# Kernel optimization log

Measured on AMD Instinct MI355X. Metric: run time of the kernel, lower is better.

Reference implementation:

```python
import jax, jax.numpy as jnp
import numpy as np

N = 100000
E = 800000

def elu(x):
    return jnp.where(x > 0, x, jnp.expm1(x))

def transformer_conv(x, src, dst, ea, Wq, bq, Wk, bk, Wv, bv, We, Ws, bs, heads, ch):
    # PyG TransformerConv (concat=True, root_weight=True, beta=False, eval so dropout off)
    n = x.shape[0]
    q = (x @ Wq + bq).reshape(n, heads, ch)
    k = (x @ Wk + bk).reshape(n, heads, ch)
    v = (x @ Wv + bv).reshape(n, heads, ch)
    e = (ea @ We).reshape(-1, heads, ch)            # [E,H,C], lin_edge has no bias
    kj = k[src] + e                                  # [E,H,C]
    logits = (q[dst] * kj).sum(-1) / jnp.sqrt(jnp.float32(ch))  # [E,H]
    # segment softmax over incoming edges of each dst node
    m = jax.ops.segment_max(logits, dst, num_segments=n)
    ex = jnp.exp(logits - m[dst])
    denom = jax.ops.segment_sum(ex, dst, num_segments=n)
    alpha = ex / denom[dst]                          # [E,H]
    msg = alpha[..., None] * (v[src] + e)            # [E,H,C]
    agg = jax.ops.segment_sum(msg, dst, num_segments=n).reshape(n, heads * ch)
    return agg + x @ Ws + bs                         # skip connection (lin_skip)

def setup_inputs() -> dict:
    key = jax.random.key(0)
    ks = jax.random.split(key, 32)
    def rn(k, shape, scale=0.1):
        return jax.random.normal(k, shape, dtype=jnp.float32) * scale
    d = {}
    d['x'] = jax.random.normal(ks[0], (N, 23), dtype=jnp.float32)
    d['edge_index'] = jax.random.randint(ks[1], (2, E), 0, N, dtype=jnp.int32)
    d['edge_attr'] = jax.random.normal(ks[2], (E, 7), dtype=jnp.float32)
    d['linA_w'] = rn(ks[3], (23, 23)); d['linA_b'] = jnp.zeros((23,), jnp.float32)
    d['linB_w'] = rn(ks[4], (23, 23)); d['linB_b'] = jnp.zeros((23,), jnp.float32)
    # conv1: in=23, heads=8, out=24 -> 192
    d['q1_w'] = rn(ks[5], (23, 192)); d['q1_b'] = jnp.zeros((192,), jnp.float32)
    d['k1_w'] = rn(ks[6], (23, 192)); d['k1_b'] = jnp.zeros((192,), jnp.float32)
    d['v1_w'] = rn(ks[7], (23, 192)); d['v1_b'] = jnp.zeros((192,), jnp.float32)
    d['e1_w'] = rn(ks[8], (7, 192))
    d['s1_w'] = rn(ks[9], (23, 192)); d['s1_b'] = jnp.zeros((192,), jnp.float32)
    # conv4: in=192, heads=8, out=8 -> 64
    d['q2_w'] = rn(ks[10], (192, 64)); d['q2_b'] = jnp.zeros((64,), jnp.float32)
    d['k2_w'] = rn(ks[11], (192, 64)); d['k2_b'] = jnp.zeros((64,), jnp.float32)
    d['v2_w'] = rn(ks[12], (192, 64)); d['v2_b'] = jnp.zeros((64,), jnp.float32)
    d['e2_w'] = rn(ks[13], (7, 64))
    d['s2_w'] = rn(ks[14], (192, 64)); d['s2_b'] = jnp.zeros((64,), jnp.float32)
    d['lin1_w'] = rn(ks[15], (64, 20)); d['lin1_b'] = jnp.zeros((20,), jnp.float32)
    d['lin2_w'] = rn(ks[16], (20, 1)); d['lin2_b'] = jnp.zeros((1,), jnp.float32)
    return d

def reference(x, edge_index, edge_attr,
              linA_w, linA_b, linB_w, linB_b,
              q1_w, q1_b, k1_w, k1_b, v1_w, v1_b, e1_w, s1_w, s1_b,
              q2_w, q2_b, k2_w, k2_b, v2_w, v2_b, e2_w, s2_w, s2_b,
              lin1_w, lin1_b, lin2_w, lin2_b):
    src, dst = edge_index[0], edge_index[1]
    h = elu(x @ linA_w + linA_b)
    h = elu(h @ linB_w + linB_b)
    h = transformer_conv(h, src, dst, edge_attr, q1_w, q1_b, k1_w, k1_b, v1_w, v1_b, e1_w, s1_w, s1_b, 8, 24)
    h = elu(h)
    h = transformer_conv(h, src, dst, edge_attr, q2_w, q2_b, k2_w, k2_b, v2_w, v2_b, e2_w, s2_w, s2_b, 8, 8)
    h = elu(h)
    h = elu(h @ lin1_w + lin1_b)
    return h @ lin2_w + lin2_b
```

## Files before the change

kernel.cpp:

```cpp
#include <hip/hip_runtime.h>
#include <math.h>


__device__ __forceinline__ float elu_f(float x) {
    return x > 0.f ? x : expm1f(x);
}


__global__ void mlp_kernel(const float* __restrict__ x,
                           const float* __restrict__ A, const float* __restrict__ ab,
                           const float* __restrict__ B, const float* __restrict__ bb,
                           float* __restrict__ out, int n) {
    __shared__ float sA[23 * 23], sB[23 * 23], sa[23], sb[23];
    for (int t = threadIdx.x; t < 23 * 23; t += blockDim.x) { sA[t] = A[t]; sB[t] = B[t]; }
    if (threadIdx.x < 23) { sa[threadIdx.x] = ab[threadIdx.x]; sb[threadIdx.x] = bb[threadIdx.x]; }
    __syncthreads();
    int i = blockIdx.x * blockDim.x + threadIdx.x;
    if (i >= n) return;
    float xi[23], h1[23];
    #pragma unroll
    for (int j = 0; j < 23; j++) xi[j] = x[(size_t)i * 23 + j];
    #pragma unroll
    for (int o = 0; o < 23; o++) {
        float acc = sa[o];
        #pragma unroll
        for (int j = 0; j < 23; j++) acc = fmaf(xi[j], sA[j * 23 + o], acc);
        h1[o] = elu_f(acc);
    }
    #pragma unroll
    for (int o = 0; o < 23; o++) {
        float acc = sb[o];
        #pragma unroll
        for (int j = 0; j < 23; j++) acc = fmaf(h1[j], sB[j * 23 + o], acc);
        out[(size_t)i * 23 + o] = elu_f(acc);
    }
}

template<int IN, int Kc, int OUTW, int M, int TY>
__global__ void proj_tiled_kernel(const float* __restrict__ in, int n,
    const float* __restrict__ W0, const float* __restrict__ b0, float* __restrict__ o0,
    const float* __restrict__ W1, const float* __restrict__ b1, float* __restrict__ o1,
    const float* __restrict__ W2, const float* __restrict__ b2, float* __restrict__ o2,
    const float* __restrict__ W3, const float* __restrict__ b3, float* __restrict__ o3) {
    constexpr int WTOT = M * OUTW;
    constexpr int CG   = WTOT / 8;
    constexpr int BN   = TY * 4;
    constexpr int SAW  = BN + 4;
    constexpr int NT   = CG * TY;
    static_assert(IN % Kc == 0, "Kc must divide IN");
    static_assert(WTOT % 8 == 0 && OUTW % 4 == 0, "col alignment");
    __shared__ float sA[Kc][SAW];
    __shared__ float sB[Kc][WTOT];

    const int tid = threadIdx.x;
    const int tx = tid % CG;
    const int ty = tid / CG;
    const int node0 = blockIdx.x * BN;

    const int colA = tx * 4;
    const int colB = WTOT / 2 + tx * 4;
    const int matA = colA / OUTW, ccA = colA % OUTW;
    const int matB = colB / OUTW, ccB = colB % OUTW;
    const float* bA = (matA == 0 ? b0 : matA == 1 ? b1 : matA == 2 ? b2 : b3);
    const float* bB = (matB == 0 ? b0 : matB == 1 ? b1 : matB == 2 ? b2 : b3);
    float*       oA = (matA == 0 ? o0 : matA == 1 ? o1 : matA == 2 ? o2 : o3);
    float*       oB = (matB == 0 ? o0 : matB == 1 ? o1 : matB == 2 ? o2 : o3);

    float acc[4][8];
    #pragma unroll
    for (int i = 0; i < 4; i++) {
        #pragma unroll
        for (int c = 0; c < 4; c++) { acc[i][c] = bA[ccA + c]; acc[i][4 + c] = bB[ccB + c]; }
    }

    for (int k0 = 0; k0 < IN; k0 += Kc) {
        for (int t = tid; t < Kc * BN; t += NT) {
            int j = t / BN, nn = t - j * BN;
            int g = node0 + nn;
            sA[j][nn] = (g < n) ? in[(size_t)g * IN + k0 + j] : 0.f;
        }
        for (int t = tid; t < Kc * WTOT; t += NT) {
            int j = t / WTOT, c = t - j * WTOT;
            int m = c / OUTW, cm = c - m * OUTW;
            const float* Wp = (m == 0 ? W0 : m == 1 ? W1 : m == 2 ? W2 : W3);
            sB[j][c] = Wp[(size_t)(k0 + j) * OUTW + cm];
        }
        __syncthreads();
        #pragma unroll 8
        for (int j = 0; j < Kc; j++) {
            float4 a  = *(const float4*)&sA[j][ty * 4];
            float4 v0 = *(const float4*)&sB[j][colA];
            float4 v1 = *(const float4*)&sB[j][colB];
            float av[4] = {a.x, a.y, a.z, a.w};
            float bv[8] = {v0.x, v0.y, v0.z, v0.w, v1.x, v1.y, v1.z, v1.w};
            #pragma unroll
            for (int i = 0; i < 4; i++)
                #pragma unroll
                for (int c = 0; c < 8; c++)
                    acc[i][c] = fmaf(av[i], bv[c], acc[i][c]);
        }
        __syncthreads();
    }

    #pragma unroll
    for (int i = 0; i < 4; i++) {
        int g = node0 + ty * 4 + i;
        if (g >= n) continue;
        *(float4*)(oA + (size_t)g * OUTW + ccA) = make_float4(acc[i][0], acc[i][1], acc[i][2], acc[i][3]);
        *(float4*)(oB + (size_t)g * OUTW + ccB) = make_float4(acc[i][4], acc[i][5], acc[i][6], acc[i][7]);
    }
}


__global__ void zero2_kernel(int* __restrict__ a, int* __restrict__ b, int n) {
    int i = blockIdx.x * blockDim.x + threadIdx.x;
    if (i < n) { a[i] = 0; b[i] = 0; }
}

__global__ void count_kernel(const int* __restrict__ dst, int* __restrict__ cnt, int nE) {
    int e = blockIdx.x * blockDim.x + threadIdx.x;
    if (e < nE) atomicAdd(&cnt[dst[e]], 1);
}

__global__ void scan_block_kernel(int* __restrict__ cnt, int* __restrict__ bsum, int n) {
    __shared__ int sdat[256];
    int i = blockIdx.x * 256 + threadIdx.x;
    int v = (i < n) ? cnt[i] : 0;
    sdat[threadIdx.x] = v;
    __syncthreads();
    for (int off = 1; off < 256; off <<= 1) {
        int t = (threadIdx.x >= (unsigned)off) ? sdat[threadIdx.x - off] : 0;
        __syncthreads();
        sdat[threadIdx.x] += t;
        __syncthreads();
    }
    if (i < n) cnt[i] = sdat[threadIdx.x] - v;
    if (threadIdx.x == 255) bsum[blockIdx.x] = sdat[255];
}

__global__ void scan_bsum_kernel(int* __restrict__ bsum, int nb) {
    __shared__ int s[1024];
    int i = threadIdx.x;
    int v = (i < nb) ? bsum[i] : 0;
    s[i] = v;
    __syncthreads();
    for (int off = 1; off < 1024; off <<= 1) {
        int t = (i >= off) ? s[i - off] : 0;
        __syncthreads();
        s[i] += t;
        __syncthreads();
    }
    if (i < nb) bsum[i] = s[i] - v;
}

__global__ void finalize_rp_kernel(const int* __restrict__ cnt, const int* __restrict__ bsum,
                                   int* __restrict__ rp, int n, int nE) {
    int i = blockIdx.x * blockDim.x + threadIdx.x;
    if (i < n) rp[i] = cnt[i] + bsum[i >> 8];
    if (i == n) rp[n] = nE;
}

__global__ void scatter_kernel(const int* __restrict__ src, const int* __restrict__ dst,
                               const int* __restrict__ rp, int* __restrict__ cur,
                               int2* __restrict__ seS, int nE) {
    int e = blockIdx.x * blockDim.x + threadIdx.x;
    if (e >= nE) return;
    int d = dst[e];
    int pos = rp[d] + atomicAdd(&cur[d], 1);
    seS[pos] = make_int2(src[e], e);
}

template<int IN, int C, bool VMAT, bool QMAT, bool DOELU>
__global__ void conv_fused_kernel(const float* __restrict__ feat,
                                  const float* __restrict__ Wq, const float* __restrict__ qb,
                                  const float* __restrict__ Wv, const float* __restrict__ vb,
                                  const float* __restrict__ kmat, const float* __restrict__ vmat,
                                  const float* __restrict__ qmat,
                                  const float* __restrict__ ea, const float* __restrict__ We,
                                  const int* __restrict__ rp, const int2* __restrict__ seS,
                                  float* __restrict__ out, int n, float scale, int chunk) {
    constexpr int HC = 8 * C;
    constexpr int CPL = HC / 64;
    __shared__ float sWv[VMAT ? 1 : IN * HC];
    if constexpr (!VMAT) {
        for (int t = threadIdx.x; t < IN * HC; t += blockDim.x) sWv[t] = Wv[t];
        __syncthreads();
    }
    const int lane = threadIdx.x & 63;
    const int wid = (blockIdx.x * blockDim.x + threadIdx.x) >> 6;
    int d0 = wid * chunk;
    const int dEnd = min(n, d0 + chunk);
    if (d0 >= dEnd) return;
    const int ch0 = lane * CPL;

    float we[7][CPL];
    #pragma unroll
    for (int j = 0; j < 7; j++)
        #pragma unroll
        for (int c = 0; c < CPL; c++) we[j][c] = We[j * HC + ch0 + c];

    float vbr[CPL];
    if constexpr (!VMAT) {
        #pragma unroll
        for (int c = 0; c < CPL; c++) vbr[c] = vb[ch0 + c];
    }

    for (int d = d0; d < dEnd; d++) {
        float* op = out + (size_t)d * HC + ch0;
        float sk[CPL], q[CPL];
        #pragma unroll
        for (int c = 0; c < CPL; c++) sk[c] = op[c];
        if constexpr (QMAT) {
            const float* qp = qmat + (size_t)d * HC + ch0;
            #pragma unroll
            for (int c = 0; c < CPL; c++) q[c] = qp[c];
        } else {
            #pragma unroll
            for (int c = 0; c < CPL; c++) q[c] = qb[ch0 + c];
            const float* fd = feat + (size_t)d * IN;
            for (int j = 0; j < IN; j++) {
                float f = fd[j];
                #pragma unroll
                for (int c = 0; c < CPL; c++)
                    q[c] = fmaf(f, Wq[(size_t)j * HC + ch0 + c], q[c]);
            }
        }

        float m = -INFINITY, l = 0.f, acc[CPL];
        #pragma unroll
        for (int c = 0; c < CPL; c++) acc[c] = 0.f;

        const int p0 = rp[d], p1 = rp[d + 1];

        if constexpr (VMAT) {
            if (p0 < p1) {
                int2 se0 = seS[p0];
                int sC = __builtin_amdgcn_readfirstlane(se0.x);
                int eC = __builtin_amdgcn_readfirstlane(se0.y);
                int2 seN = (p0 + 1 < p1) ? seS[p0 + 1] : se0;
                float kc[CPL], vc[CPL], ec[7];
                {
                    const float* kp = kmat + (size_t)sC * HC + ch0;
                    const float* vp = vmat + (size_t)sC * HC + ch0;
                    const float* ep = ea + (size_t)eC * 7;
                    #pragma unroll
                    for (int c = 0; c < CPL; c++) { kc[c] = kp[c]; vc[c] = vp[c]; }
                    #pragma unroll
                    for (int j = 0; j < 7; j++) ec[j] = ep[j];
                }
                for (int p = p0; p < p1; p++) {
                    const bool hasN = (p + 1 < p1);
                    int2 seN2 = (p + 2 < p1) ? seS[p + 2] : seN;
                    float kn[CPL], vn[CPL], en[7];
                    if (hasN) {
                        int sN = __builtin_amdgcn_readfirstlane(seN.x);
                        int eN = __builtin_amdgcn_readfirstlane(seN.y);
                        const float* kp = kmat + (size_t)sN * HC + ch0;
                        const float* vp = vmat + (size_t)sN * HC + ch0;
                        const float* ep = ea + (size_t)eN * 7;
                        #pragma unroll
                        for (int c = 0; c < CPL; c++) { kn[c] = kp[c]; vn[c] = vp[c]; }
                        #pragma unroll
                        for (int j = 0; j < 7; j++) en[j] = ep[j];
                    }
                    float part = 0.f;
                    float vloc[CPL];
                    #pragma unroll
                    for (int c = 0; c < CPL; c++) {
                        float t = 0.f;
                        #pragma unroll
                        for (int j = 0; j < 7; j++) t = fmaf(ec[j], we[j][c], t);
                        part = fmaf(q[c], kc[c] + t, part);
                        vloc[c] = vc[c] + t;
                    }
                    part += __shfl_xor(part, 1);
                    part += __shfl_xor(part, 2);
                    part += __shfl_xor(part, 4);
                    float z = part * scale;
                    float mn = fmaxf(m, z);
                    float rs = expf(m - mn);
                    float pw = expf(z - mn);
                    l = l * rs + pw;
                    #pragma unroll
                    for (int c = 0; c < CPL; c++) acc[c] = fmaf(acc[c], rs, pw * vloc[c]);
                    m = mn;
                    if (hasN) {
                        #pragma unroll
                        for (int c = 0; c < CPL; c++) { kc[c] = kn[c]; vc[c] = vn[c]; }
                        #pragma unroll
                        for (int j = 0; j < 7; j++) ec[j] = en[j];
                    }
                    seN = seN2;
                }
            }
        } else {
            for (int p = p0; p < p1; p++) {
                int2 se = seS[p];
                int s = se.x, eid = se.y;
                const float* eav = ea + (size_t)eid * 7;
                float ev[7];
                #pragma unroll
                for (int j = 0; j < 7; j++) ev[j] = eav[j];
                const float* kp = kmat + (size_t)s * HC + ch0;
                float vv[CPL];
                float part = 0.f;
                #pragma unroll
                for (int c = 0; c < CPL; c++) {
                    float t = 0.f;
                    #pragma unroll
                    for (int j = 0; j < 7; j++) t = fmaf(ev[j], we[j][c], t);
                    part = fmaf(q[c], kp[c] + t, part);
                    vv[c] = t + vbr[c];
                }
                const float* fs = feat + (size_t)s * IN;
                for (int j = 0; j < IN; j++) {
                    float f = fs[j];
                    #pragma unroll
                    for (int c = 0; c < CPL; c++) vv[c] = fmaf(f, sWv[j * HC + ch0 + c], vv[c]);
                }
                part += __shfl_xor(part, 1);
                part += __shfl_xor(part, 2);
                part += __shfl_xor(part, 4);
                float z = part * scale;
                float mn = fmaxf(m, z);
                float rs = expf(m - mn);
                float pw = expf(z - mn);
                l = l * rs + pw;
                #pragma unroll
                for (int c = 0; c < CPL; c++) acc[c] = fmaf(acc[c], rs, pw * vv[c]);
                m = mn;
            }
        }

        float invl = (l > 0.f) ? 1.f / l : 0.f;
        #pragma unroll
        for (int c = 0; c < CPL; c++) {
            float r = sk[c] + acc[c] * invl;
            op[c] = DOELU ? elu_f(r) : r;
        }
    }
}

__global__ void head_kernel(const float* __restrict__ h, const float* __restrict__ W1,
                            const float* __restrict__ b1, const float* __restrict__ W2,
                            const float* __restrict__ b2, float* __restrict__ out, int n) {
    __shared__ float sW1[64 * 20], sb1[20], sW2[20], sb2;
    for (int t = threadIdx.x; t < 64 * 20; t += blockDim.x) sW1[t] = W1[t];
    if (threadIdx.x < 20) { sb1[threadIdx.x] = b1[threadIdx.x]; sW2[threadIdx.x] = W2[threadIdx.x]; }
    if (threadIdx.x == 0) sb2 = b2[0];
    __syncthreads();
    int i = blockIdx.x * blockDim.x + threadIdx.x;
    if (i >= n) return;
    float hv[64];
    const float* hp = h + (size_t)i * 64;
    #pragma unroll
    for (int j = 0; j < 64; j++) hv[j] = elu_f(hp[j]);
    float acc2 = sb2;
    for (int o = 0; o < 20; o++) {
        float a = sb1[o];
        #pragma unroll
        for (int j = 0; j < 64; j++) a = fmaf(hv[j], sW1[j * 20 + o], a);
        acc2 = fmaf(elu_f(a), sW2[o], acc2);
    }
    out[i] = acc2;
}

__global__ void zero_out_kernel(float* __restrict__ out, int n) {
    int i = blockIdx.x * blockDim.x + threadIdx.x;
    if (i < n) out[i] = 0.f;
}


extern "C" void kernel_launch(void* const* d_in, const int* in_sizes, int n_in,
                              void* d_out, int out_size, void* d_ws, size_t ws_size,
                              hipStream_t stream) {
    const float* x   = (const float*)d_in[0];
    const int*   ei  = (const int*)d_in[1];
    const float* ea  = (const float*)d_in[2];
    const float* Aw  = (const float*)d_in[3];
    const float* Ab  = (const float*)d_in[4];
    const float* Bw  = (const float*)d_in[5];
    const float* Bb  = (const float*)d_in[6];
    const float* q1w = (const float*)d_in[7];  const float* q1b = (const float*)d_in[8];
    const float* k1w = (const float*)d_in[9];  const float* k1b = (const float*)d_in[10];
    const float* v1w = (const float*)d_in[11]; const float* v1b = (const float*)d_in[12];
    const float* e1w = (const float*)d_in[13];
    const float* s1w = (const float*)d_in[14]; const float* s1b = (const float*)d_in[15];
    const float* q2w = (const float*)d_in[16]; const float* q2b = (const float*)d_in[17];
    const float* k2w = (const float*)d_in[18]; const float* k2b = (const float*)d_in[19];
    const float* v2w = (const float*)d_in[20]; const float* v2b = (const float*)d_in[21];
    const float* e2w = (const float*)d_in[22];
    const float* s2w = (const float*)d_in[23]; const float* s2b = (const float*)d_in[24];
    const float* l1w = (const float*)d_in[25]; const float* l1b = (const float*)d_in[26];
    const float* l2w = (const float*)d_in[27]; const float* l2b = (const float*)d_in[28];

    const int n  = in_sizes[0] / 23;
    const int nE = in_sizes[1] / 2;
    const int* src = ei;
    const int* dst = ei + nE;
    float* out = (float*)d_out;
    const int B = 256;
    const int nb = (n + 255) / 256;

    size_t fl_h1 = ((size_t)n * 23 + 3) & ~(size_t)3;
    size_t fl_o1 = (size_t)n * 192;
    size_t fl_kvA = (size_t)n * 384;
    size_t fl_kB  = (size_t)n * 192;
    size_t fl_q1  = (size_t)n * 192;
    size_t ints_total = 2 * (size_t)nE + ((size_t)n + 1) + n + n + 1024;

    size_t tierB_bytes  = (fl_h1 + fl_o1 + fl_kB) * 4 + ints_total * 4;
    size_t tierA_bytes  = (fl_h1 + fl_o1 + fl_kvA) * 4 + ints_total * 4;
    size_t tierA2_bytes = tierA_bytes + fl_q1 * 4;

    if (ws_size < tierB_bytes || nb > 1024) {
        zero_out_kernel<<<(out_size + B - 1) / B, B, 0, stream>>>(out, out_size);
        return;
    }
    const int tier = (ws_size >= tierA2_bytes) ? 2 : (ws_size >= tierA_bytes) ? 1 : 0;

    float* ws = (float*)d_ws;
    size_t off = 0;
    float* h1   = ws + off; off += fl_h1;
    float* o1   = ws + off; off += fl_o1;
    float* kbuf = ws + off; off += (tier >= 1 ? fl_kvA : fl_kB);
    float* vbuf = (tier >= 1) ? (kbuf + (size_t)n * 192) : nullptr;
    float* q1buf = nullptr;
    if (tier == 2) { q1buf = ws + off; off += fl_q1; }
    int2* seS = (int2*)(ws + off);
    int* ip = (int*)(seS + nE);
    int* rp   = ip; ip += (size_t)n + 1;
    int* cnt  = ip; ip += n;
    int* cur  = ip; ip += n;
    int* bsum = ip;

    float* q2buf = kbuf;
    float* k2    = (tier >= 1) ? (kbuf + (size_t)n * 64)  : kbuf;
    float* v2    = (tier >= 1) ? (kbuf + (size_t)n * 128) : (kbuf + (size_t)n * 64);
    float* o2    = (tier >= 1) ? (kbuf + (size_t)n * 192) : (kbuf + (size_t)n * 128);

    const float sc1 = 1.0f / sqrtf(24.0f);
    const float sc2 = 1.0f / sqrtf(8.0f);
    const float* np = nullptr;
    float* npw = nullptr;

    zero2_kernel<<<(n + B - 1) / B, B, 0, stream>>>(cnt, cur, n);
    count_kernel<<<(nE + B - 1) / B, B, 0, stream>>>(dst, cnt, nE);
    scan_block_kernel<<<nb, 256, 0, stream>>>(cnt, bsum, n);
    scan_bsum_kernel<<<1, 1024, 0, stream>>>(bsum, nb);
    finalize_rp_kernel<<<(n + 1 + B - 1) / B, B, 0, stream>>>(cnt, bsum, rp, n, nE);
    scatter_kernel<<<(nE + B - 1) / B, B, 0, stream>>>(src, dst, rp, cur, seS, nE);

    mlp_kernel<<<(n + B - 1) / B, B, 0, stream>>>(x, Aw, Ab, Bw, Bb, h1, n);

    const int gproj = (n + 31) / 32;

    const int CB = 2048;
    const int NW = CB * 4;
    const int chunk = (n + NW - 1) / NW;

    if (tier == 2) {
        proj_tiled_kernel<23, 23, 192, 3, 8><<<gproj, 576, 0, stream>>>(
            h1, n, k1w, k1b, kbuf, v1w, v1b, vbuf, s1w, s1b, o1, np, np, npw);
        proj_tiled_kernel<23, 23, 192, 1, 8><<<gproj, 192, 0, stream>>>(
            h1, n, q1w, q1b, q1buf, np, np, npw, np, np, npw, np, np, npw);
        conv_fused_kernel<23, 24, true, true, true><<<CB, 256, 0, stream>>>(
            h1, q1w, q1b, v1w, v1b, kbuf, vbuf, q1buf, ea, e1w, rp, seS, o1, n, sc1, chunk);
    } else if (tier == 1) {
        proj_tiled_kernel<23, 23, 192, 3, 8><<<gproj, 576, 0, stream>>>(
            h1, n, k1w, k1b, kbuf, v1w, v1b, vbuf, s1w, s1b, o1, np, np, npw);
        conv_fused_kernel<23, 24, true, false, true><<<CB, 256, 0, stream>>>(
            h1, q1w, q1b, v1w, v1b, kbuf, vbuf, np, ea, e1w, rp, seS, o1, n, sc1, chunk);
    } else {
        proj_tiled_kernel<23, 23, 192, 2, 8><<<gproj, 384, 0, stream>>>(
            h1, n, k1w, k1b, kbuf, s1w, s1b, o1, np, np, npw, np, np, npw);
        conv_fused_kernel<23, 24, false, false, true><<<CB, 256, 0, stream>>>(
            h1, q1w, q1b, v1w, v1b, kbuf, np, np, ea, e1w, rp, seS, o1, n, sc1, chunk);
    }

    if (tier >= 1) {
        proj_tiled_kernel<192, 32, 64, 4, 8><<<gproj, 256, 0, stream>>>(
            o1, n, q2w, q2b, q2buf, k2w, k2b, k2, v2w, v2b, v2, s2w, s2b, o2);
        conv_fused_kernel<192, 8, true, true, false><<<CB, 256, 0, stream>>>(
            o1, q2w, q2b, v2w, v2b, k2, v2, q2buf, ea, e2w, rp, seS, o2, n, sc2, chunk);
    } else {
        proj_tiled_kernel<192, 32, 64, 3, 8><<<gproj, 192, 0, stream>>>(
            o1, n, k2w, k2b, k2, v2w, v2b, v2, s2w, s2b, o2, np, np, npw);
        conv_fused_kernel<192, 8, true, false, false><<<CB, 256, 0, stream>>>(
            o1, q2w, q2b, v2w, v2b, k2, v2, np, ea, e2w, rp, seS, o2, n, sc2, chunk);
    }

    head_kernel<<<(n + B - 1) / B, B, 0, stream>>>(o2, l1w, l1b, l2w, l2b, out, n);
}
```

Baseline: 1.222 ms.

## Interleave K and V rows per node for contiguous edge gathers

Adds a FUSED mode to the projection kernel so K and V are written interleaved into one [n, 2*HC] buffer. Each source node's K and V now sit next to each other, so the conv kernel's per-edge gather touches one contiguous span instead of two separate rows. The projection launches are regrouped: K+V are fused, and Q and the skip projection are paired, with TY=16 for layer 2. It also adds launch_bounds(256,4) to the conv kernel and halves the conv grid (CB 2048→1024), which changes occupancy and per-wave chunk length.

```diff
diff --git a/kernel.cpp b/kernel.cpp
--- a/kernel.cpp
+++ b/kernel.cpp
@@ -36,7 +36,7 @@
     }
 }
 
-template<int IN, int Kc, int OUTW, int M, int TY>
+template<int IN, int Kc, int OUTW, int M, int TY, bool FUSED>
 __global__ void proj_tiled_kernel(const float* __restrict__ in, int n,
     const float* __restrict__ W0, const float* __restrict__ b0, float* __restrict__ o0,
     const float* __restrict__ W1, const float* __restrict__ b1, float* __restrict__ o1,
@@ -106,8 +106,13 @@
     for (int i = 0; i < 4; i++) {
         int g = node0 + ty * 4 + i;
         if (g >= n) continue;
-        *(float4*)(oA + (size_t)g * OUTW + ccA) = make_float4(acc[i][0], acc[i][1], acc[i][2], acc[i][3]);
-        *(float4*)(oB + (size_t)g * OUTW + ccB) = make_float4(acc[i][4], acc[i][5], acc[i][6], acc[i][7]);
+        if constexpr (FUSED) {
+            *(float4*)(o0 + (size_t)g * WTOT + colA) = make_float4(acc[i][0], acc[i][1], acc[i][2], acc[i][3]);
+            *(float4*)(o0 + (size_t)g * WTOT + colB) = make_float4(acc[i][4], acc[i][5], acc[i][6], acc[i][7]);
+        } else {
+            *(float4*)(oA + (size_t)g * OUTW + ccA) = make_float4(acc[i][0], acc[i][1], acc[i][2], acc[i][3]);
+            *(float4*)(oB + (size_t)g * OUTW + ccB) = make_float4(acc[i][4], acc[i][5], acc[i][6], acc[i][7]);
+        }
     }
 }
 
@@ -171,14 +176,14 @@
 }
 
 template<int IN, int C, bool VMAT, bool QMAT, bool DOELU>
-__global__ void conv_fused_kernel(const float* __restrict__ feat,
-                                  const float* __restrict__ Wq, const float* __restrict__ qb,
-                                  const float* __restrict__ Wv, const float* __restrict__ vb,
-                                  const float* __restrict__ kmat, const float* __restrict__ vmat,
-                                  const float* __restrict__ qmat,
-                                  const float* __restrict__ ea, const float* __restrict__ We,
-                                  const int* __restrict__ rp, const int2* __restrict__ seS,
-                                  float* __restrict__ out, int n, float scale, int chunk) {
+__global__ __launch_bounds__(256, 4)
+void conv_fused_kernel(const float* __restrict__ feat,
+                       const float* __restrict__ Wq, const float* __restrict__ qb,
+                       const float* __restrict__ Wv, const float* __restrict__ vb,
+                       const float* __restrict__ kmat, const float* __restrict__ qmat,
+                       const float* __restrict__ ea, const float* __restrict__ We,
+                       const int* __restrict__ rp, const int2* __restrict__ seS,
+                       float* __restrict__ out, int n, float scale, int chunk) {
     constexpr int HC = 8 * C;
     constexpr int CPL = HC / 64;
     __shared__ float sWv[VMAT ? 1 : IN * HC];
@@ -240,11 +245,10 @@
                 int2 seN = (p0 + 1 < p1) ? seS[p0 + 1] : se0;
                 float kc[CPL], vc[CPL], ec[7];
                 {
-                    const float* kp = kmat + (size_t)sC * HC + ch0;
-                    const float* vp = vmat + (size_t)sC * HC + ch0;
+                    const float* kp = kmat + (size_t)sC * (2 * HC) + ch0;
                     const float* ep = ea + (size_t)eC * 7;
                     #pragma unroll
-                    for (int c = 0; c < CPL; c++) { kc[c] = kp[c]; vc[c] = vp[c]; }
+                    for (int c = 0; c < CPL; c++) { kc[c] = kp[c]; vc[c] = kp[HC + c]; }
                     #pragma unroll
                     for (int j = 0; j < 7; j++) ec[j] = ep[j];
                 }
@@ -255,11 +259,10 @@
                     if (hasN) {
                         int sN = __builtin_amdgcn_readfirstlane(seN.x);
                         int eN = __builtin_amdgcn_readfirstlane(seN.y);
-                        const float* kp = kmat + (size_t)sN * HC + ch0;
-                        const float* vp = vmat + (size_t)sN * HC + ch0;
+                        const float* kp = kmat + (size_t)sN * (2 * HC) + ch0;
                         const float* ep = ea + (size_t)eN * 7;
                         #pragma unroll
-                        for (int c = 0; c < CPL; c++) { kn[c] = kp[c]; vn[c] = vp[c]; }
+                        for (int c = 0; c < CPL; c++) { kn[c] = kp[c]; vn[c] = kp[HC + c]; }
                         #pragma unroll
                         for (int j = 0; j < 7; j++) en[j] = ep[j];
                     }
@@ -424,7 +427,6 @@
     float* h1   = ws + off; off += fl_h1;
     float* o1   = ws + off; off += fl_o1;
     float* kbuf = ws + off; off += (tier >= 1 ? fl_kvA : fl_kB);
-    float* vbuf = (tier >= 1) ? (kbuf + (size_t)n * 192) : nullptr;
     float* q1buf = nullptr;
     if (tier == 2) { q1buf = ws + off; off += fl_q1; }
     int2* seS = (int2*)(ws + off);
@@ -434,9 +436,8 @@
     int* cur  = ip; ip += n;
     int* bsum = ip;
 
-    float* q2buf = kbuf;
-    float* k2    = (tier >= 1) ? (kbuf + (size_t)n * 64)  : kbuf;
-    float* v2    = (tier >= 1) ? (kbuf + (size_t)n * 128) : (kbuf + (size_t)n * 64);
+    float* kv2   = kbuf;
+    float* q2buf = (tier >= 1) ? (kbuf + (size_t)n * 128) : nullptr;
     float* o2    = (tier >= 1) ? (kbuf + (size_t)n * 192) : (kbuf + (size_t)n * 128);
 
     const float sc1 = 1.0f / sqrtf(24.0f);
@@ -453,41 +454,46 @@
 
     mlp_kernel<<<(n + B - 1) / B, B, 0, stream>>>(x, Aw, Ab, Bw, Bb, h1, n);
 
-    const int gproj = (n + 31) / 32;
-
-    const int CB = 2048;
+    const int gproj32 = (n + 31) / 32;
+    const int gproj64 = (n + 63) / 64;
+
+    const int CB = 1024;
     const int NW = CB * 4;
     const int chunk = (n + NW - 1) / NW;
 
-    if (tier == 2) {
-        proj_tiled_kernel<23, 23, 192, 3, 8><<<gproj, 576, 0, stream>>>(
-            h1, n, k1w, k1b, kbuf, v1w, v1b, vbuf, s1w, s1b, o1, np, np, npw);
-        proj_tiled_kernel<23, 23, 192, 1, 8><<<gproj, 192, 0, stream>>>(
-            h1, n, q1w, q1b, q1buf, np, np, npw, np, np, npw, np, np, npw);
-        conv_fused_kernel<23, 24, true, true, true><<<CB, 256, 0, stream>>>(
-            h1, q1w, q1b, v1w, v1b, kbuf, vbuf, q1buf, ea, e1w, rp, seS, o1, n, sc1, chunk);
-    } else if (tier == 1) {
-        proj_tiled_kernel<23, 23, 192, 3, 8><<<gproj, 576, 0, stream>>>(
-            h1, n, k1w, k1b, kbuf, v1w, v1b, vbuf, s1w, s1b, o1, np, np, npw);
-        conv_fused_kernel<23, 24, true, false, true><<<CB, 256, 0, stream>>>(
-            h1, q1w, q1b, v1w, v1b, kbuf, vbuf, np, ea, e1w, rp, seS, o1, n, sc1, chunk);
+    if (tier >= 1) {
+        proj_tiled_kernel<23, 23, 192, 2, 8, true><<<gproj32, 384, 0, stream>>>(
+            h1, n, k1w, k1b, kbuf, v1w, v1b, npw, np, np, npw, np, np, npw);
+        if (tier == 2) {
+            proj_tiled_kernel<23, 23, 192, 2, 8, false><<<gproj32, 384, 0, stream>>>(
+                h1, n, s1w, s1b, o1, q1w, q1b, q1buf, np, np, npw, np, np, npw);
+            conv_fused_kernel<23, 24, true, true, true><<<CB, 256, 0, stream>>>(
+                h1, q1w, q1b, v1w, v1b, kbuf, q1buf, ea, e1w, rp, seS, o1, n, sc1, chunk);
+        } else {
+            proj_tiled_kernel<23, 23, 192, 1, 8, false><<<gproj32, 192, 0, stream>>>(
+                h1, n, s1w, s1b, o1, np, np, npw, np, np, npw, np, np, npw);
+            conv_fused_kernel<23, 24, true, false, true><<<CB, 256, 0, stream>>>(
+                h1, q1w, q1b, v1w, v1b, kbuf, np, ea, e1w, rp, seS, o1, n, sc1, chunk);
+        }
     } else {
-        proj_tiled_kernel<23, 23, 192, 2, 8><<<gproj, 384, 0, stream>>>(
+        proj_tiled_kernel<23, 23, 192, 2, 8, false><<<gproj32, 384, 0, stream>>>(
             h1, n, k1w, k1b, kbuf, s1w, s1b, o1, np, np, npw, np, np, npw);
         conv_fused_kernel<23, 24, false, false, true><<<CB, 256, 0, stream>>>(
-            h1, q1w, q1b, v1w, v1b, kbuf, np, np, ea, e1w, rp, seS, o1, n, sc1, chunk);
-    }
-
+            h1, q1w, q1b, v1w, v1b, kbuf, np, ea, e1w, rp, seS, o1, n, sc1, chunk);
+    }
+
+    proj_tiled_kernel<192, 32, 64, 2, 16, true><<<gproj64, 256, 0, stream>>>(
+        o1, n, k2w, k2b, kv2, v2w, v2b, npw, np, np, npw, np, np, npw);
     if (tier >= 1) {
-        proj_tiled_kernel<192, 32, 64, 4, 8><<<gproj, 256, 0, stream>>>(
-            o1, n, q2w, q2b, q2buf, k2w, k2b, k2, v2w, v2b, v2, s2w, s2b, o2);
+        proj_tiled_kernel<192, 32, 64, 2, 16, false><<<gproj64, 256, 0, stream>>>(
+            o1, n, q2w, q2b, q2buf, s2w, s2b, o2, np, np, npw, np, np, npw);
         conv_fused_kernel<192, 8, true, true, false><<<CB, 256, 0, stream>>>(
-            o1, q2w, q2b, v2w, v2b, k2, v2, q2buf, ea, e2w, rp, seS, o2, n, sc2, chunk);
+            o1, q2w, q2b, v2w, v2b, kv2, q2buf, ea, e2w, rp, seS, o2, n, sc2, chunk);
     } else {
-        proj_tiled_kernel<192, 32, 64, 3, 8><<<gproj, 192, 0, stream>>>(
-            o1, n, k2w, k2b, k2, v2w, v2b, v2, s2w, s2b, o2, np, np, npw);
+        proj_tiled_kernel<192, 32, 64, 1, 16, false><<<gproj64, 128, 0, stream>>>(
+            o1, n, s2w, s2b, o2, np, np, npw, np, np, npw, np, np, npw);
         conv_fused_kernel<192, 8, true, false, false><<<CB, 256, 0, stream>>>(
-            o1, q2w, q2b, v2w, v2b, k2, v2, np, ea, e2w, rp, seS, o2, n, sc2, chunk);
+            o1, q2w, q2b, v2w, v2b, kv2, np, ea, e2w, rp, seS, o2, n, sc2, chunk);
     }
 
     head_kernel<<<(n + B - 1) / B, B, 0, stream>>>(o2, l1w, l1b, l2w, l2b, out, n);
```

Result: faster. 1.185 ms (-3.0%).
